# Optimization experiments

Hardware: AMD Instinct MI355X
Metric: run time of the kernel (lower is better)

Reference implementation:

```python
import jax, jax.numpy as jnp
import numpy as np

L = 4          # n_layers
HID = 64       # hidden_channels
MODES = 16     # n_modes
HEADS = 4      # n_heads
NP_SP = 500    # spatial engram patterns
NP_FR = 200    # spectral engram patterns
ED = 8         # embed_dim
WS = 4         # spatial window size
PRIME = 31.0


def setup_inputs() -> dict:
    key = jax.random.key(0)
    ks = jax.random.split(key, 20)
    B, Cin, Cout, S = 16, 3, 1, 16384
    f = lambda k, sh: jax.random.normal(k, sh, dtype=jnp.float32) * 0.05
    ch = HID // HEADS
    return {
        "x": jax.random.normal(ks[0], (B, Cin, S), dtype=jnp.float32),
        "lift_W": f(ks[1], (Cin, HID)), "lift_b": f(ks[2], (HID,)),
        "proj_W": f(ks[3], (HID, Cout)), "proj_b": f(ks[4], (Cout,)),
        "sp_emb": f(ks[5], (L, NP_SP, ED)), "sp_W": f(ks[6], (L, ED, HID)), "sp_b": f(ks[7], (L, HID)),
        "fr_emb": f(ks[8], (L, NP_FR, ED)), "fr_W": f(ks[9], (L, ED, HID * MODES)), "fr_b": f(ks[10], (L, HID * MODES)),
        "g_W1": f(ks[11], (L, 3 * HID, 64)), "g_b1": f(ks[12], (L, 64)),
        "g_W2": f(ks[13], (L, 64, 3)), "g_b2": f(ks[14], (L, 3)),
        "mhf_Wr": f(ks[15], (L, HEADS, ch, ch, MODES)),
        "mhf_Wi": f(ks[16], (L, HEADS, ch, ch, MODES)),
    }


def _spatial_engram(x, emb, W, b):
    # x: [B, C, S] -> hash each replicate-padded window of size WS -> embedding gather -> linear
    B, C, S = x.shape
    pad = WS // 2
    xp = jnp.pad(x, ((0, 0), (0, 0), (pad, pad)), mode='edge')   # [B, C, S+WS]
    sC = xp.sum(axis=1)                                          # [B, S+WS]
    # window sum over WS consecutive positions (vectorized over all seq positions)
    wsum = sC[:, 0:S] + sC[:, 1:S + 1] + sC[:, 2:S + 2] + sC[:, 3:S + 3]  # [B, S]
    idx = (wsum * PRIME).astype(jnp.int32) % NP_SP               # truncate-toward-zero like torch .long()
    idx = jnp.clip(idx, 0, NP_SP - 1)
    e = emb[idx]                                                 # [B, S, ED] gather
    out = e @ W + b                                              # [B, S, C]
    return out.transpose(0, 2, 1)                                # [B, C, S]


def _spectral_engram(x, emb, W, b):
    B, C, S = x.shape
    xf = jnp.fft.rfft(x, axis=-1)                                # [B, C, F]
    mag = jnp.abs(xf[:, :, :MODES]).mean(axis=1)                 # [B, MODES]
    idx = ((mag * 1000.0).astype(jnp.int32)).sum(axis=1) % NP_FR # [B]
    e = emb[idx]                                                 # [B, ED]
    proj = (e @ W + b).reshape(B, C, MODES)
    full = jnp.zeros((B, C, xf.shape[-1]), dtype=xf.dtype).at[:, :, :MODES].set(proj.astype(xf.dtype))
    return jnp.fft.irfft(full, n=S, axis=-1)


def _mhf_spectral_conv(x, Wr, Wi):
    # multi-head Fourier spectral conv: per-head complex channel mixing on low modes
    B, C, S = x.shape
    ch = C // HEADS
    xf = jnp.fft.rfft(x, axis=-1)                                # [B, C, F]
    xh = xf[:, :, :MODES].reshape(B, HEADS, ch, MODES)           # [B, H, ch, M]
    Wc = Wr + 1j * Wi                                            # [H, ch, ch, M]
    of = jnp.einsum('bhim,hiom->bhom', xh, Wc).reshape(B, C, MODES)
    full = jnp.zeros((B, C, xf.shape[-1]), dtype=xf.dtype).at[:, :, :MODES].set(of)
    return jnp.fft.irfft(full, n=S, axis=-1)


def _gated_fusion(sp, mh, fr, W1, b1, W2, b2):
    g = jnp.concatenate([sp.mean(-1), mh.mean(-1), fr.mean(-1)], axis=-1)  # [B, 3C]
    h = jax.nn.relu(g @ W1 + b1)
    w = jax.nn.softmax(h @ W2 + b2, axis=-1)                     # [B, 3]
    return (w[:, 0, None, None] * sp + w[:, 1, None, None] * mh + w[:, 2, None, None] * fr)


def reference(x, lift_W, lift_b, proj_W, proj_b, sp_emb, sp_W, sp_b,
              fr_emb, fr_W, fr_b, g_W1, g_b1, g_W2, g_b2, mhf_Wr, mhf_Wi):
    # lifting: [B, Cin, S] -> [B, HID, S]
    h = jnp.einsum('bcs,cd->bds', x, lift_W) + lift_b[None, :, None]
    for i in range(L):
        sp = _spatial_engram(h, sp_emb[i], sp_W[i], sp_b[i])
        mh = _mhf_spectral_conv(h, mhf_Wr[i], mhf_Wi[i])
        fr = _spectral_engram(h, fr_emb[i], fr_W[i], fr_b[i])
        h = _gated_fusion(sp, mh, fr, g_W1[i], g_b1[i], g_W2[i], g_b2[i])
        h = jax.nn.gelu(h, approximate=False)  # torch F.gelu default = exact erf
    out = jnp.einsum('bcs,cd->bds', h, proj_W) + proj_b[None, :, None]
    return out
```

## Files before the change

kernel.cpp:

```cpp
#include <hip/hip_runtime.h>
#include <math.h>

#define B_ 16
#define CIN_ 3
#define HID_ 64
#define S_ 16384
#define MODES_ 16
#define HEADS_ 4
#define CH_ 16
#define ED_ 8
#define NPSP_ 500
#define NPFR_ 200
#define LAYERS_ 4
#define RECW_ 42

__device__ __forceinline__ double gelu_exact(double v) {
    double y = v * 0.70710678118654752440;
    double t = y * y;
    double p = -1.2290555301717926e-09;
    p = fma(p, t, 1.4807192815879218e-08);
    p = fma(p, t, -1.6365838718281893e-07);
    p = fma(p, t, 1.6462114365889246e-06);
    p = fma(p, t, -1.4925650358406251e-05);
    p = fma(p, t, 1.2055332981789664e-04);
    p = fma(p, t, -8.5483270234508528e-04);
    p = fma(p, t, 5.2239776254421878e-03);
    p = fma(p, t, -2.6866170645131252e-02);
    p = fma(p, t, 1.1283791670955126e-01);
    p = fma(p, t, -3.7612638903183752e-01);
    p = fma(p, t, 1.1283791670955126e+00);
    double er = y * p;
    if (t > 0.5000001) er = erf(y);
    return 0.5 * v * (1.0 + er);
}

__device__ __constant__ double KC_[16] = {1.0, 0.99518472667219688624,
    0.98078528040323044913, 0.95694033573220886494, 0.92387953251128675613,
    0.88192126434835502971, 0.83146961230254523708, 0.77301045336273696081,
    0.70710678118654752440, 0.63439328416364549822, 0.55557023301960222474,
    0.47139673682599764856, 0.38268343236508977173, 0.29028467725446236764,
    0.19509032201612826785, 0.09801714032956060199};
__device__ __constant__ double KS_[16] = {0.0, 0.09801714032956060199,
    0.19509032201612826785, 0.29028467725446236764, 0.38268343236508977173,
    0.47139673682599764856, 0.55557023301960222474, 0.63439328416364549822,
    0.70710678118654752440, 0.77301045336273696081, 0.83146961230254523708,
    0.88192126434835502971, 0.92387953251128675613, 0.95694033573220886494,
    0.98078528040323044913, 0.99518472667219688624};

__global__ __launch_bounds__(256) void k_lift(const float* __restrict__ x,
                                              const float* __restrict__ W,
                                              const float* __restrict__ bias,
                                              float* __restrict__ h,
                                              double* __restrict__ sC2) {
    int b = blockIdx.y;
    int s = blockIdx.x * 256 + threadIdx.x;
    const float* xb = x + (size_t)b * CIN_ * S_ + s;
    double x0 = (double)xb[0];
    double x1 = (double)xb[S_];
    double x2 = (double)xb[2 * S_];
    float* hb = h + (size_t)b * HID_ * S_ + s;
    double accA = 0.0, accB = 0.0;
    for (int d = 0; d < HID_; ++d) {
        double v = x0 * (double)W[d];
        v = fma(x1, (double)W[HID_ + d], v);
        v = fma(x2, (double)W[2 * HID_ + d], v);
        v += (double)bias[d];
        hb[(size_t)d * S_] = (float)v;
        if (d < 32) accA += v; else accB += v;
    }
    sC2[(size_t)b * S_ + s] = accA;
    sC2[(size_t)(B_ + b) * S_ + s] = accB;
}

__global__ __launch_bounds__(256) void k_hash(const double* __restrict__ sC2,
                                              const float* __restrict__ emb_l,
                                              int* __restrict__ idx,
                                              double* __restrict__ Eb) {
    int b = blockIdx.y;
    int s0 = blockIdx.x * 256;
    int t = threadIdx.x;
    __shared__ double sl[260];
    for (int j = t; j < 260; j += 256) {
        int p = s0 - 2 + j;
        p = p < 0 ? 0 : (p > S_ - 1 ? S_ - 1 : p);
        sl[j] = sC2[(size_t)b * S_ + p] + sC2[(size_t)(B_ + b) * S_ + p];
    }
    __syncthreads();
    double wsum = ((sl[t] + sl[t + 1]) + sl[t + 2]) + sl[t + 3];
    int ti = (int)(wsum * 31.0);
    int id = ti % NPSP_;
    if (id < 0) id += NPSP_;
    idx[(size_t)b * S_ + s0 + t] = id;

    const float* er = emb_l + id * ED_;
    double ev[8];
#pragma unroll
    for (int k = 0; k < 8; k++) ev[k] = (double)er[k];

    int lane = t & 63, wv = t >> 6;
    __shared__ double red[4][8];
#pragma unroll
    for (int k = 0; k < 8; k++) {
        double v = ev[k];
        for (int off = 32; off > 0; off >>= 1) v += __shfl_down(v, off, 64);
        if (lane == 0) red[wv][k] = v;
    }
    __syncthreads();
    if (t < 8) {
        double v = red[0][t] + red[1][t] + red[2][t] + red[3][t];
        atomicAdd(&Eb[b * ED_ + t], v);
    }
}

__global__ __launch_bounds__(256, 2) void k_dft(const float* __restrict__ h,
                                                double* __restrict__ Xr,
                                                double* __restrict__ Xi) {
    int b = blockIdx.y;
    int c0 = blockIdx.x * 2;
    int t = threadIdx.x;
    const float* h0 = h + ((size_t)(b * HID_ + c0)) * S_ + t;
    const float* h1 = h0 + S_;

    double acc[64];
#pragma unroll
    for (int k = 0; k < 64; k++) acc[k] = 0.0;

    double cmv[16], smv[16];
    cmv[0] = 1.0; smv[0] = 0.0;
    cmv[1] = cospi((double)t / 8192.0);
    smv[1] = sinpi((double)t / 8192.0);
#pragma unroll
    for (int m = 2; m < 16; m++) {
        cmv[m] = cmv[m - 1] * cmv[1] - smv[m - 1] * smv[1];
        smv[m] = smv[m - 1] * cmv[1] + cmv[m - 1] * smv[1];
    }

    for (int k = 0; k < 16; k++) {
        int s = k << 8;
        double a0 = (double)h0[s];
        double b0 = (double)h0[s + 4096];
        double c0v = (double)h0[s + 8192];
        double d0 = (double)h0[s + 12288];
        double a1 = (double)h1[s];
        double b1 = (double)h1[s + 4096];
        double c1v = (double)h1[s + 8192];
        double d1 = (double)h1[s + 12288];

        double t10 = a0 + c0v, t20 = b0 + d0;
        double g00 = t10 + t20, g20 = t10 - t20;
        double ar0 = a0 - c0v, br0 = b0 - d0;
        double t11 = a1 + c1v, t21 = b1 + d1;
        double g01 = t11 + t21, g21 = t11 - t21;
        double ar1 = a1 - c1v, br1 = b1 - d1;

        acc[0] += g00;
        acc[32] += g01;
#pragma unroll
        for (int m = 1; m < 16; m++) {
            double c = cmv[m], s_ = smv[m];
            if ((m & 1) == 0) {
                double g0x = (m & 2) ? g20 : g00;
                double g1x = (m & 2) ? g21 : g01;
                acc[m]      = fma(g0x, c,  acc[m]);
                acc[16 + m] = fma(g0x, s_, acc[16 + m]);
                acc[32 + m] = fma(g1x, c,  acc[32 + m]);
                acc[48 + m] = fma(g1x, s_, acc[48 + m]);
            } else if ((m & 2) == 0) {
                acc[m]      = fma(ar0, c,  fma(-br0, s_, acc[m]));
                acc[16 + m] = fma(ar0, s_, fma( br0, c,  acc[16 + m]));
                acc[32 + m] = fma(ar1, c,  fma(-br1, s_, acc[32 + m]));
                acc[48 + m] = fma(ar1, s_, fma( br1, c,  acc[48 + m]));
            } else {
                acc[m]      = fma(ar0, c,  fma( br0, s_, acc[m]));
                acc[16 + m] = fma(ar0, s_, fma(-br0, c,  acc[16 + m]));
                acc[32 + m] = fma(ar1, c,  fma( br1, s_, acc[32 + m]));
                acc[48 + m] = fma(ar1, s_, fma(-br1, c,  acc[48 + m]));
            }
        }
#pragma unroll
        for (int m = 1; m < 16; m++) {
            double cn = cmv[m] * KC_[m] - smv[m] * KS_[m];
            double sn = smv[m] * KC_[m] + cmv[m] * KS_[m];
            cmv[m] = cn; smv[m] = sn;
        }
    }

    int lane = t & 63, wv = t >> 6;
    __shared__ double red[4][64];
#pragma unroll
    for (int k = 0; k < 64; k++) {
        double v = acc[k];
        for (int off = 32; off > 0; off >>= 1) v += __shfl_down(v, off, 64);
        if (lane == 0) red[wv][k] = v;
    }
    __syncthreads();
    if (t < 64) {
        double v = red[0][t] + red[1][t] + red[2][t] + red[3][t];
        int cc = t >> 5, im = (t >> 4) & 1, m = t & 15;
        size_t o = ((size_t)b * HID_ + c0 + cc) * MODES_ + m;
        if (im) Xi[o] = -v;
        else    Xr[o] = v;
    }
}

__global__ __launch_bounds__(256) void k_gate(const double* __restrict__ Xr,
                                              const double* __restrict__ Xi,
                                              const float* __restrict__ mWr,
                                              const float* __restrict__ mWi,
                                              const float* __restrict__ fr_emb_l,
                                              const float* __restrict__ fr_W_l,
                                              const float* __restrict__ fr_b_l,
                                              const double* __restrict__ Eb,
                                              const float* __restrict__ sp_W_l,
                                              const float* __restrict__ sp_b_l,
                                              const float* __restrict__ gW1,
                                              const float* __restrict__ gb1,
                                              const float* __restrict__ gW2,
                                              const float* __restrict__ gb2,
                                              double* __restrict__ RECg) {
    int b = blockIdx.x;
    int t = threadIdx.x;
    __shared__ double sXr[1024], sXi[1024];
    __shared__ double sMr[1024], sMi[1024], sP[1024];
    __shared__ double gg[192], h1s[64], sww[3];
    __shared__ int magI[MODES_];
    __shared__ int fidxS;

    for (int j = t; j < 1024; j += 256) {
        sXr[j] = Xr[(size_t)b * 1024 + j];
        sXi[j] = Xi[(size_t)b * 1024 + j];
    }
    __syncthreads();

    if (t < MODES_) {
        double acc = 0.0;
        for (int c = 0; c < HID_; c++) {
            double re = sXr[c * MODES_ + t];
            double im = sXi[c * MODES_ + t];
            acc += sqrt(re * re + im * im);
        }
        magI[t] = (int)(acc * (1.0 / 64.0) * 1000.0);
    }

    for (int u = t; u < 1024; u += 256) {
        int hh = u >> 8, rem = u & 255, o = rem >> 4, m = rem & 15;
        const float* wr = mWr + (size_t)hh * CH_ * CH_ * MODES_;
        const float* wi = mWi + (size_t)hh * CH_ * CH_ * MODES_;
        double aR = 0.0, aI = 0.0;
#pragma unroll 4
        for (int i = 0; i < CH_; i++) {
            double xrv = sXr[(hh * CH_ + i) * MODES_ + m];
            double xiv = sXi[(hh * CH_ + i) * MODES_ + m];
            double wrv = (double)wr[(i * CH_ + o) * MODES_ + m];
            double wiv = (double)wi[(i * CH_ + o) * MODES_ + m];
            aR += xrv * wrv - xiv * wiv;
            aI += xrv * wiv + xiv * wrv;
        }
        sMr[(hh * CH_ + o) * MODES_ + m] = aR;
        sMi[(hh * CH_ + o) * MODES_ + m] = aI;
    }
    __syncthreads();

    if (t == 0) {
        int ssum = 0;
        for (int m = 0; m < MODES_; m++) ssum += magI[m];
        int f = ssum % NPFR_;
        if (f < 0) f += NPFR_;
        fidxS = f;
    }
    __syncthreads();

    {
        const float* fe = fr_emb_l + fidxS * ED_;
        for (int u = t; u < 1024; u += 256) {
            double acc = 0.0;
            for (int e = 0; e < ED_; e++)
                acc += (double)fe[e] * (double)fr_W_l[e * 1024 + u];
            sP[u] = acc + (double)fr_b_l[u];
        }
    }
    __syncthreads();

    if (t < 64) {
        double a = 0.0;
        for (int e = 0; e < ED_; e++)
            a += Eb[b * ED_ + e] * (double)sp_W_l[e * 64 + t];
        gg[t]       = a * (1.0 / 16384.0) + (double)sp_b_l[t];
        gg[64 + t]  = sMr[t * MODES_] * (1.0 / 16384.0);
        gg[128 + t] = sP[t * MODES_] * (1.0 / 16384.0);
    }
    __syncthreads();
    if (t < 64) {
        double a = 0.0;
        for (int k = 0; k < 192; k++) a += gg[k] * (double)gW1[k * 64 + t];
        a += (double)gb1[t];
        h1s[t] = a > 0.0 ? a : 0.0;
    }
    __syncthreads();
    if (t == 0) {
        double l[3];
        for (int j = 0; j < 3; j++) {
            double a = 0.0;
            for (int k = 0; k < 64; k++) a += h1s[k] * (double)gW2[k * 3 + j];
            l[j] = a + (double)gb2[j];
        }
        double mx = fmax(l[0], fmax(l[1], l[2]));
        double e0 = exp(l[0] - mx), e1 = exp(l[1] - mx), e2 = exp(l[2] - mx);
        double sum = e0 + e1 + e2;
        sww[0] = e0 / sum; sww[1] = e1 / sum; sww[2] = e2 / sum;
    }
    __syncthreads();

    double w0s = sww[0], w1s = sww[1], w2s = sww[2];
    double* R = RECg + (size_t)b * HID_ * RECW_;
    for (int u = t; u < 1024; u += 256) {
        int c = u >> 4, m = u & 15;
        double km = (m == 0 ? 1.0 : 2.0) * (1.0 / 16384.0);
        R[c * RECW_ + 2 * m]     = km * (w1s * sMr[u] + w2s * sP[u]);
        R[c * RECW_ + 2 * m + 1] = (m == 0) ? 0.0 : -(km * w1s * sMi[u]);
    }
    for (int u = t; u < 512; u += 256) {
        int e = u >> 6, c = u & 63;
        R[c * RECW_ + 32 + e] = w0s * (double)sp_W_l[u];
    }
    if (t < 64) {
        R[t * RECW_ + 40] = w0s * (double)sp_b_l[t];
        R[t * RECW_ + 41] = 0.0;
    }
}

__global__ __launch_bounds__(256) void k_recon(const int* __restrict__ idx,
                                               const float* __restrict__ sp_emb_l,
                                               const double* __restrict__ RECg,
                                               float* __restrict__ h,
                                               double* __restrict__ sC2) {
    int b = blockIdx.y;
    int cz = blockIdx.z;
    int cbase = cz * 32;
    int s1 = blockIdx.x * 256 + threadIdx.x;
    int s2 = s1 + 8192;
    int t = threadIdx.x;
    __shared__ double rec[32 * RECW_];
    __shared__ float semb[NPSP_ * 9];
    for (int j = t; j < 32 * RECW_; j += 256)
        rec[j] = RECg[(size_t)b * HID_ * RECW_ + cbase * RECW_ + j];
    for (int j = t; j < NPSP_ * 8; j += 256) {
        int r = j >> 3, e2i = j & 7;
        semb[r * 9 + e2i] = sp_emb_l[j];
    }
    __syncthreads();

    int id1 = idx[(size_t)b * S_ + s1];
    int id2 = idx[(size_t)b * S_ + s2];
    double e1[8], e2[8];
#pragma unroll
    for (int k = 0; k < 8; k++) e1[k] = (double)semb[id1 * 9 + k];
#pragma unroll
    for (int k = 0; k < 8; k++) e2[k] = (double)semb[id2 * 9 + k];

    double cb = cospi((double)s1 / 8192.0);
    double sb = sinpi((double)s1 / 8192.0);
    double cm[16], sm[16];
    cm[0] = 1.0; sm[0] = 0.0;
    cm[1] = cb;  sm[1] = sb;
#pragma unroll
    for (int m = 2; m < 16; m++) {
        cm[m] = cm[m - 1] * cb - sm[m - 1] * sb;
        sm[m] = sm[m - 1] * cb + cm[m - 1] * sb;
    }

    float* hb = h + (size_t)b * HID_ * S_ + (size_t)cbase * S_;
    double cs1 = 0.0, cs2 = 0.0;
    for (int c = 0; c < 32; c++) {
        const double2* r2 = (const double2*)(rec + c * RECW_);
        double base = rec[c * RECW_ + 40];
        double p1 = base, p2 = base;
#pragma unroll
        for (int k = 0; k < 4; k++) {
            double2 w = r2[16 + k];
            p1 = fma(e1[2 * k], w.x, p1);
            p1 = fma(e1[2 * k + 1], w.y, p1);
            p2 = fma(e2[2 * k], w.x, p2);
            p2 = fma(e2[2 * k + 1], w.y, p2);
        }
        double vE = 0.0, vO = 0.0;
#pragma unroll
        for (int m = 0; m < 16; m += 2) {
            double2 qe = r2[m];
            double2 qo = r2[m + 1];
            vE = fma(qe.x, cm[m], vE);
            vE = fma(qe.y, sm[m], vE);
            vO = fma(qo.x, cm[m + 1], vO);
            vO = fma(qo.y, sm[m + 1], vO);
        }
        double g1 = gelu_exact(p1 + (vE + vO));
        double g2 = gelu_exact(p2 + (vE - vO));
        hb[(size_t)c * S_ + s1] = (float)g1;
        hb[(size_t)c * S_ + s2] = (float)g2;
        cs1 += g1;
        cs2 += g2;
    }
    sC2[(size_t)(cz * B_ + b) * S_ + s1] = cs1;
    sC2[(size_t)(cz * B_ + b) * S_ + s2] = cs2;
}

__global__ __launch_bounds__(256) void k_proj(const float* __restrict__ h,
                                              const float* __restrict__ pW,
                                              const float* __restrict__ pb,
                                              float* __restrict__ out) {
    int b = blockIdx.y;
    int s = blockIdx.x * 256 + threadIdx.x;
    const float* hb = h + (size_t)b * HID_ * S_ + s;
    double acc = 0.0;
    for (int d = 0; d < HID_; d++)
        acc += (double)hb[(size_t)d * S_] * (double)pW[d];
    out[(size_t)b * S_ + s] = (float)(acc + (double)pb[0]);
}

extern "C" void kernel_launch(void* const* d_in, const int* in_sizes, int n_in,
                              void* d_out, int out_size, void* d_ws, size_t ws_size,
                              hipStream_t stream) {
    const float* x      = (const float*)d_in[0];
    const float* lift_W = (const float*)d_in[1];
    const float* lift_b = (const float*)d_in[2];
    const float* proj_W = (const float*)d_in[3];
    const float* proj_b = (const float*)d_in[4];
    const float* sp_emb = (const float*)d_in[5];
    const float* sp_W   = (const float*)d_in[6];
    const float* sp_b   = (const float*)d_in[7];
    const float* fr_emb = (const float*)d_in[8];
    const float* fr_W   = (const float*)d_in[9];
    const float* fr_b   = (const float*)d_in[10];
    const float* g_W1   = (const float*)d_in[11];
    const float* g_b1   = (const float*)d_in[12];
    const float* g_W2   = (const float*)d_in[13];
    const float* g_b2   = (const float*)d_in[14];
    const float* mhf_Wr = (const float*)d_in[15];
    const float* mhf_Wi = (const float*)d_in[16];

    char* ws = (char*)d_ws;
    float* h    = (float*)ws;   ws += (size_t)B_ * HID_ * S_ * 4;
    double* sC2 = (double*)ws;  ws += (size_t)2 * B_ * S_ * 8;
    int* idx    = (int*)ws;     ws += (size_t)B_ * S_ * 4;
    double* Xr  = (double*)ws;  ws += (size_t)B_ * HID_ * MODES_ * 8;
    double* Xi  = (double*)ws;  ws += (size_t)B_ * HID_ * MODES_ * 8;
    double* REC = (double*)ws;  ws += (size_t)B_ * HID_ * RECW_ * 8;
    double* Eb  = (double*)ws;  ws += (size_t)LAYERS_ * B_ * ED_ * 8;

    hipMemsetAsync(Eb, 0, (size_t)LAYERS_ * B_ * ED_ * 8, stream);

    dim3 blk(256);
    k_lift<<<dim3(S_ / 256, B_), blk, 0, stream>>>(x, lift_W, lift_b, h, sC2);

    for (int lay = 0; lay < LAYERS_; ++lay) {
        k_hash<<<dim3(S_ / 256, B_), blk, 0, stream>>>(
            sC2, sp_emb + (size_t)lay * NPSP_ * ED_, idx, Eb + (size_t)lay * B_ * ED_);
        k_dft<<<dim3(HID_ / 2, B_), blk, 0, stream>>>(h, Xr, Xi);
        k_gate<<<dim3(B_), blk, 0, stream>>>(
            Xr, Xi,
            mhf_Wr + (size_t)lay * HEADS_ * CH_ * CH_ * MODES_,
            mhf_Wi + (size_t)lay * HEADS_ * CH_ * CH_ * MODES_,
            fr_emb + (size_t)lay * NPFR_ * ED_,
            fr_W + (size_t)lay * ED_ * HID_ * MODES_,
            fr_b + (size_t)lay * HID_ * MODES_,
            Eb + (size_t)lay * B_ * ED_,
            sp_W + (size_t)lay * ED_ * HID_,
            sp_b + (size_t)lay * HID_,
            g_W1 + (size_t)lay * 192 * 64,
            g_b1 + (size_t)lay * 64,
            g_W2 + (size_t)lay * 64 * 3,
            g_b2 + (size_t)lay * 3,
            REC);
        k_recon<<<dim3(S_ / 512, B_, 2), blk, 0, stream>>>(
            idx, sp_emb + (size_t)lay * NPSP_ * ED_, REC, h, sC2);
    }

    k_proj<<<dim3(S_ / 256, B_), blk, 0, stream>>>(h, proj_W, proj_b, (float*)d_out);
}
```

Measured before the change: 595.6 us.

## Exploit quarter-period twiddle symmetry to reconstruct four positions per thread

The reconstruction kernel now computes four sequence positions per thread (s, s+N/4, s+N/2, s+3N/4), using the symmetry of cos/sin at quarter-period shifts to share the 16-mode inverse DFT partial sums across all four outputs. This roughly halves the per-output double-precision FMA work for the spectral part and halves the number of blocks that reload the shared rec table and embedding table. The embedding table load is vectorized with float4, and launch bounds request 2 blocks per CU. Register pressure rises with four embedding vectors and accumulators, and the grid halves, which may reduce occupancy or latency hiding.

```diff
diff --git a/kernel.cpp b/kernel.cpp
--- a/kernel.cpp
+++ b/kernel.cpp
@@ -329,37 +329,45 @@
     }
 }
 
-__global__ __launch_bounds__(256) void k_recon(const int* __restrict__ idx,
-                                               const float* __restrict__ sp_emb_l,
-                                               const double* __restrict__ RECg,
-                                               float* __restrict__ h,
-                                               double* __restrict__ sC2) {
+__global__ __launch_bounds__(256, 2) void k_recon(const int* __restrict__ idx,
+                                                  const float* __restrict__ sp_emb_l,
+                                                  const double* __restrict__ RECg,
+                                                  float* __restrict__ h,
+                                                  double* __restrict__ sC2) {
     int b = blockIdx.y;
     int cz = blockIdx.z;
     int cbase = cz * 32;
-    int s1 = blockIdx.x * 256 + threadIdx.x;
-    int s2 = s1 + 8192;
+    int s0 = blockIdx.x * 256 + threadIdx.x;
     int t = threadIdx.x;
     __shared__ double rec[32 * RECW_];
     __shared__ float semb[NPSP_ * 9];
     for (int j = t; j < 32 * RECW_; j += 256)
         rec[j] = RECg[(size_t)b * HID_ * RECW_ + cbase * RECW_ + j];
-    for (int j = t; j < NPSP_ * 8; j += 256) {
-        int r = j >> 3, e2i = j & 7;
-        semb[r * 9 + e2i] = sp_emb_l[j];
-    }
-    __syncthreads();
-
-    int id1 = idx[(size_t)b * S_ + s1];
-    int id2 = idx[(size_t)b * S_ + s2];
-    double e1[8], e2[8];
-#pragma unroll
-    for (int k = 0; k < 8; k++) e1[k] = (double)semb[id1 * 9 + k];
-#pragma unroll
-    for (int k = 0; k < 8; k++) e2[k] = (double)semb[id2 * 9 + k];
-
-    double cb = cospi((double)s1 / 8192.0);
-    double sb = sinpi((double)s1 / 8192.0);
+    for (int j4 = t; j4 < NPSP_ * 2; j4 += 256) {
+        float4 v = reinterpret_cast<const float4*>(sp_emb_l)[j4];
+        int r = j4 >> 1, e0 = (j4 & 1) * 4;
+        semb[r * 9 + e0]     = v.x;
+        semb[r * 9 + e0 + 1] = v.y;
+        semb[r * 9 + e0 + 2] = v.z;
+        semb[r * 9 + e0 + 3] = v.w;
+    }
+    __syncthreads();
+
+    int id0 = idx[(size_t)b * S_ + s0];
+    int id1 = idx[(size_t)b * S_ + s0 + 4096];
+    int id2 = idx[(size_t)b * S_ + s0 + 8192];
+    int id3 = idx[(size_t)b * S_ + s0 + 12288];
+    double e0v[8], e1v[8], e2v[8], e3v[8];
+#pragma unroll
+    for (int k = 0; k < 8; k++) {
+        e0v[k] = (double)semb[id0 * 9 + k];
+        e1v[k] = (double)semb[id1 * 9 + k];
+        e2v[k] = (double)semb[id2 * 9 + k];
+        e3v[k] = (double)semb[id3 * 9 + k];
+    }
+
+    double cb = cospi((double)s0 / 8192.0);
+    double sb = sinpi((double)s0 / 8192.0);
     double cm[16], sm[16];
     cm[0] = 1.0; sm[0] = 0.0;
     cm[1] = cb;  sm[1] = sb;
@@ -370,38 +378,47 @@
     }
 
     float* hb = h + (size_t)b * HID_ * S_ + (size_t)cbase * S_;
-    double cs1 = 0.0, cs2 = 0.0;
+    double cs0 = 0.0, cs1 = 0.0, cs2 = 0.0, cs3 = 0.0;
     for (int c = 0; c < 32; c++) {
         const double2* r2 = (const double2*)(rec + c * RECW_);
         double base = rec[c * RECW_ + 40];
-        double p1 = base, p2 = base;
+        double p0 = base, p1 = base, p2 = base, p3 = base;
 #pragma unroll
         for (int k = 0; k < 4; k++) {
             double2 w = r2[16 + k];
-            p1 = fma(e1[2 * k], w.x, p1);
-            p1 = fma(e1[2 * k + 1], w.y, p1);
-            p2 = fma(e2[2 * k], w.x, p2);
-            p2 = fma(e2[2 * k + 1], w.y, p2);
-        }
-        double vE = 0.0, vO = 0.0;
-#pragma unroll
-        for (int m = 0; m < 16; m += 2) {
-            double2 qe = r2[m];
-            double2 qo = r2[m + 1];
-            vE = fma(qe.x, cm[m], vE);
-            vE = fma(qe.y, sm[m], vE);
-            vO = fma(qo.x, cm[m + 1], vO);
-            vO = fma(qo.y, sm[m + 1], vO);
-        }
-        double g1 = gelu_exact(p1 + (vE + vO));
-        double g2 = gelu_exact(p2 + (vE - vO));
-        hb[(size_t)c * S_ + s1] = (float)g1;
-        hb[(size_t)c * S_ + s2] = (float)g2;
-        cs1 += g1;
-        cs2 += g2;
-    }
-    sC2[(size_t)(cz * B_ + b) * S_ + s1] = cs1;
-    sC2[(size_t)(cz * B_ + b) * S_ + s2] = cs2;
+            p0 = fma(e0v[2 * k], w.x, p0); p0 = fma(e0v[2 * k + 1], w.y, p0);
+            p1 = fma(e1v[2 * k], w.x, p1); p1 = fma(e1v[2 * k + 1], w.y, p1);
+            p2 = fma(e2v[2 * k], w.x, p2); p2 = fma(e2v[2 * k + 1], w.y, p2);
+            p3 = fma(e3v[2 * k], w.x, p3); p3 = fma(e3v[2 * k + 1], w.y, p3);
+        }
+        double PA = 0.0, PB = 0.0, PC = 0.0, PD = 0.0, QB = 0.0, QD = 0.0;
+#pragma unroll
+        for (int mm = 0; mm < 16; mm += 4) {
+            double2 q0 = r2[mm], q1 = r2[mm + 1], q2 = r2[mm + 2], q3 = r2[mm + 3];
+            PA = fma(q0.x, cm[mm], PA);     PA = fma(q0.y, sm[mm], PA);
+            PB = fma(q1.x, cm[mm + 1], PB); PB = fma(q1.y, sm[mm + 1], PB);
+            QB = fma(q1.y, cm[mm + 1], QB); QB = fma(-q1.x, sm[mm + 1], QB);
+            PC = fma(q2.x, cm[mm + 2], PC); PC = fma(q2.y, sm[mm + 2], PC);
+            PD = fma(q3.x, cm[mm + 3], PD); PD = fma(q3.y, sm[mm + 3], PD);
+            QD = fma(q3.y, cm[mm + 3], QD); QD = fma(-q3.x, sm[mm + 3], QD);
+        }
+        double u0 = PA + PC, u1 = PA - PC;
+        double w0 = PB + PD, qd = QB - QD;
+        double g0 = gelu_exact(p0 + (u0 + w0));
+        double g1 = gelu_exact(p1 + (u1 + qd));
+        double g2 = gelu_exact(p2 + (u0 - w0));
+        double g3 = gelu_exact(p3 + (u1 - qd));
+        hb[(size_t)c * S_ + s0]         = (float)g0;
+        hb[(size_t)c * S_ + s0 + 4096]  = (float)g1;
+        hb[(size_t)c * S_ + s0 + 8192]  = (float)g2;
+        hb[(size_t)c * S_ + s0 + 12288] = (float)g3;
+        cs0 += g0; cs1 += g1; cs2 += g2; cs3 += g3;
+    }
+    double* sc = sC2 + (size_t)(cz * B_ + b) * S_;
+    sc[s0]         = cs0;
+    sc[s0 + 4096]  = cs1;
+    sc[s0 + 8192]  = cs2;
+    sc[s0 + 12288] = cs3;
 }
 
 __global__ __launch_bounds__(256) void k_proj(const float* __restrict__ h,
@@ -471,7 +488,7 @@
             g_W2 + (size_t)lay * 64 * 3,
             g_b2 + (size_t)lay * 3,
             REC);
-        k_recon<<<dim3(S_ / 512, B_, 2), blk, 0, stream>>>(
+        k_recon<<<dim3(S_ / 1024, B_, 2), blk, 0, stream>>>(
             idx, sp_emb + (size_t)lay * NPSP_ * ED_, REC, h, sC2);
     }
 
```

Measured after the change: 569.0 us. 4.5% less time.
